# Optimization experiments

Measured on AMD Instinct MI355X. Metric: run time of the kernel, lower is better.

## Reference

```python
import math
import jax, jax.numpy as jnp
import numpy as np

B, N_COLS, CHANNELS, NUM_HEADS = 512, 128, 512, 8
D_HEAD = CHANNELS // NUM_HEADS


def setup_inputs() -> dict:
    key = jax.random.key(0)
    ks = jax.random.split(key, 9)
    s = 1.0 / math.sqrt(CHANNELS)
    x = jax.random.normal(ks[0], (B, N_COLS, CHANNELS), dtype=jnp.float32)
    Wq = jax.random.uniform(ks[1], (CHANNELS, CHANNELS), jnp.float32, -s, s)
    bq = jax.random.uniform(ks[2], (CHANNELS,), jnp.float32, -s, s)
    Wk = jax.random.uniform(ks[3], (CHANNELS, CHANNELS), jnp.float32, -s, s)
    bk = jax.random.uniform(ks[4], (CHANNELS,), jnp.float32, -s, s)
    Wv = jax.random.uniform(ks[5], (CHANNELS, CHANNELS), jnp.float32, -s, s)
    bv = jax.random.uniform(ks[6], (CHANNELS,), jnp.float32, -s, s)
    Wo = jax.random.uniform(ks[7], (CHANNELS, CHANNELS), jnp.float32, -s, s)
    bo = jax.random.uniform(ks[8], (CHANNELS,), jnp.float32, -s, s)
    return {"x": x, "Wq": Wq, "bq": bq, "Wk": Wk, "bk": bk,
            "Wv": Wv, "bv": bv, "Wo": Wo, "bo": bo}


def reference(x, Wq, bq, Wk, bk, Wv, bv, Wo, bo):
    b, n, c = x.shape
    h, d = NUM_HEADS, D_HEAD

    def split_heads(t):  # [b, n, c] -> [b, h, n, d]
        return t.reshape(b, n, h, d).transpose(0, 2, 1, 3)

    Q = split_heads(x @ Wq + bq)
    K = split_heads(x @ Wk + bk)
    V = split_heads(x @ Wv + bv)

    # raw scores [b, h, q, k]
    scores = jnp.einsum('bhqd,bhkd->bhqk', Q, K)
    # causal mask over columns; note: mask added BEFORE scaling by sqrt(d)
    causal = jnp.tril(jnp.ones((n, n), dtype=jnp.float32))
    mask = (1.0 - causal) * -100000.0
    attn = jax.nn.softmax((scores + mask) / math.sqrt(d), axis=-1)
    out = jnp.einsum('bhqk,bhkd->bhqd', attn, V)
    out = out.transpose(0, 2, 1, 3).reshape(b, n, c)
    return out @ Wo + bo
```

## Files before the change

### kernel.cpp

```cpp
#include <hip/hip_runtime.h>

typedef _Float16 f16;
typedef _Float16 half8 __attribute__((ext_vector_type(8)));
typedef _Float16 half4 __attribute__((ext_vector_type(4)));
typedef float f32x4 __attribute__((ext_vector_type(4)));

#define B_SZ 512
#define NQ   128
#define CH   512
#define NH   8
#define DH   64
#define MTOK (B_SZ*NQ)
#define KD   512

#define MFMA16(a,b,c) __builtin_amdgcn_mfma_f32_16x16x32_f16((a),(b),(c),0,0,0)

#define GLDS16(g,l) __builtin_amdgcn_global_load_lds( \
    (__attribute__((address_space(1))) void*)(g), \
    (__attribute__((address_space(3))) void*)(l), 16, 0, 0)

__global__ __launch_bounds__(256) void k_cvt(const float* __restrict__ x,
                                             f16* __restrict__ xb) {
  const int n8 = MTOK * KD / 8;
  int i = blockIdx.x * blockDim.x + threadIdx.x;
  const int stride = gridDim.x * blockDim.x;
  for (; i < n8; i += stride) {
    f32x4 a = ((const f32x4*)x)[2 * i];
    f32x4 b = ((const f32x4*)x)[2 * i + 1];
    half8 h;
    h[0] = (f16)a[0]; h[1] = (f16)a[1]; h[2] = (f16)a[2]; h[3] = (f16)a[3];
    h[4] = (f16)b[0]; h[5] = (f16)b[1]; h[6] = (f16)b[2]; h[7] = (f16)b[3];
    ((half8*)xb)[i] = h;
  }
}

__global__ __launch_bounds__(256) void k_wt(const float* __restrict__ Wq,
                                            const float* __restrict__ Wk,
                                            const float* __restrict__ Wv,
                                            const float* __restrict__ Wo,
                                            f16* __restrict__ wt) {
  const int n = blockIdx.x;
  const float* W = (n < 512) ? Wq : (n < 1024) ? Wk : (n < 1536) ? Wv : Wo;
  const int c = n & 511;
  for (int k = threadIdx.x; k < 512; k += blockDim.x)
    wt[n * 512 + k] = (f16)W[k * 512 + c];
}

__global__ __launch_bounds__(256, 4) void k_qkv(
    const f16* __restrict__ A, const f16* __restrict__ Bw,
    const float* __restrict__ bq, const float* __restrict__ bk,
    const float* __restrict__ bv,
    f16* __restrict__ qb, f16* __restrict__ kb, f16* __restrict__ vb) {
  __shared__ f16 la[128 * 32];
  __shared__ f16 lb[128 * 32];
  const int tid = threadIdx.x;
  const int w = tid >> 6, lane = tid & 63;
  const int ln = lane & 15, g = lane >> 4;
  const int wr = w >> 1, wc = w & 1;
  const int s = blockIdx.x >> 3;
  const int ml = s / 12;
  const int ntile = s - ml * 12;
  const int mtile = (blockIdx.x & 7) * 64 + ml;

  const int srow = w * 16 + (lane >> 2);
  const int scol = ((lane & 3) ^ ((lane >> 3) & 3)) * 8;
  const f16* gA = A + (mtile * 128 + srow) * KD + scol;
  const f16* gB = Bw + (ntile * 128 + srow) * KD + scol;
  f16* lA = la + w * 512;
  f16* lB = lb + w * 512;
  const int slotx = (g ^ ((ln >> 1) & 3)) * 8;

  f32x4 acc[4][4] = {};

  for (int kt = 0; kt < 16; ++kt) {
    const int k0 = kt * 32;
    GLDS16(gA + k0, lA);
    GLDS16(gA + 64 * KD + k0, lA + 2048);
    GLDS16(gB + k0, lB);
    GLDS16(gB + 64 * KD + k0, lB + 2048);
    __syncthreads();
    half8 af[4], bf[4];
#pragma unroll
    for (int m = 0; m < 4; ++m)
      af[m] = *(const half8*)(la + (wr * 64 + m * 16 + ln) * 32 + slotx);
#pragma unroll
    for (int n = 0; n < 4; ++n)
      bf[n] = *(const half8*)(lb + (wc * 64 + n * 16 + ln) * 32 + slotx);
#pragma unroll
    for (int m = 0; m < 4; ++m)
#pragma unroll
      for (int n = 0; n < 4; ++n)
        acc[m][n] = MFMA16(af[m], bf[n], acc[m][n]);
    __syncthreads();
  }

  const int b = mtile;
  const int colbase = ntile * 128 + wc * 64;
#pragma unroll
  for (int m = 0; m < 4; ++m) {
    const int nn0 = wr * 64 + m * 16 + g * 4;
#pragma unroll
    for (int n = 0; n < 4; ++n) {
      const int col = colbase + n * 16 + ln;
      const int which = col >> 9;
      const int c = col & 511;
      const int h = c >> 6, d = c & 63;
      const float bias = (which == 0) ? bq[c] : (which == 1) ? bk[c] : bv[c];
      if (which < 2) {
        f16* dst = ((which == 0) ? qb : kb) + ((b * NH + h) * NQ + nn0) * DH + d;
#pragma unroll
        for (int r = 0; r < 4; ++r)
          dst[r * DH] = (f16)(acc[m][n][r] + bias);
      } else {
        half4 v4;
#pragma unroll
        for (int r = 0; r < 4; ++r)
          v4[r] = (f16)(acc[m][n][r] + bias);
        *(half4*)(vb + ((b * NH + h) * DH + d) * NQ + nn0) = v4;
      }
    }
  }
}

__global__ __launch_bounds__(256, 2) void k_attn(
    const f16* __restrict__ qbuf, const f16* __restrict__ kbuf,
    const f16* __restrict__ vbuf, f16* __restrict__ ao) {
  __shared__ f16 kl[128 * 72];
  __shared__ f16 vl[64 * 136];
  __shared__ f16 pl[128 * 136];
  const int bh = blockIdx.x;
  const f16* Qp = qbuf + bh * (NQ * DH);
  const f16* Kp = kbuf + bh * (NQ * DH);
  const f16* Vp = vbuf + bh * (DH * NQ);
  const int tid = threadIdx.x;
  const int w = tid >> 6, lane = tid & 63;
  const int ln = lane & 15, g = lane >> 4;

#pragma unroll
  for (int i = 0; i < 4; ++i) {
    const int e = i * 2048 + tid * 8;
    *(half8*)(kl + (e >> 6) * 72 + (e & 63)) = *(const half8*)(Kp + e);
  }
#pragma unroll
  for (int i = 0; i < 4; ++i) {
    const int e = i * 2048 + tid * 8;
    *(half8*)(vl + (e >> 7) * 136 + (e & 127)) = *(const half8*)(Vp + e);
  }
  half8 qf[2][2];
#pragma unroll
  for (int m = 0; m < 2; ++m)
#pragma unroll
    for (int ks = 0; ks < 2; ++ks)
      qf[m][ks] = *(const half8*)(Qp + (w * 32 + m * 16 + ln) * DH + ks * 32 + g * 8);
  __syncthreads();

  f32x4 s[2][8] = {};
#pragma unroll
  for (int ks = 0; ks < 2; ++ks)
#pragma unroll
    for (int n = 0; n < 8; ++n) {
      half8 kf = *(const half8*)(kl + (n * 16 + ln) * 72 + ks * 32 + g * 8);
      s[0][n] = MFMA16(qf[0][ks], kf, s[0][n]);
      s[1][n] = MFMA16(qf[1][ks], kf, s[1][n]);
    }

  float inv[2][4];
#pragma unroll
  for (int m = 0; m < 2; ++m) {
#pragma unroll
    for (int r = 0; r < 4; ++r) {
      const int q = w * 32 + m * 16 + g * 4 + r;
      float z[8];
      float rm = -1e30f;
#pragma unroll
      for (int n = 0; n < 8; ++n) {
        const int col = n * 16 + ln;
        float zz = s[m][n][r] * 0.125f + ((col > q) ? -12500.0f : 0.0f);
        z[n] = zz;
        rm = fmaxf(rm, zz);
      }
      rm = fmaxf(rm, __shfl_xor(rm, 1));
      rm = fmaxf(rm, __shfl_xor(rm, 2));
      rm = fmaxf(rm, __shfl_xor(rm, 4));
      rm = fmaxf(rm, __shfl_xor(rm, 8));
      float rs = 0.f;
#pragma unroll
      for (int n = 0; n < 8; ++n) {
        const float p = __expf(z[n] - rm);
        rs += p;
        pl[q * 136 + n * 16 + ln] = (f16)p;
      }
      rs += __shfl_xor(rs, 1);
      rs += __shfl_xor(rs, 2);
      rs += __shfl_xor(rs, 4);
      rs += __shfl_xor(rs, 8);
      inv[m][r] = 1.0f / rs;
    }
  }

  f32x4 o[2][4] = {};
#pragma unroll
  for (int ks = 0; ks < 4; ++ks) {
    half8 pf0 = *(const half8*)(pl + (w * 32 + ln) * 136 + ks * 32 + g * 8);
    half8 pf1 = *(const half8*)(pl + (w * 32 + 16 + ln) * 136 + ks * 32 + g * 8);
#pragma unroll
    for (int n = 0; n < 4; ++n) {
      half8 vf = *(const half8*)(vl + (n * 16 + ln) * 136 + ks * 32 + g * 8);
      o[0][n] = MFMA16(pf0, vf, o[0][n]);
      o[1][n] = MFMA16(pf1, vf, o[1][n]);
    }
  }

  const int b = bh >> 3, h = bh & 7;
  f16* dst = ao + (b * NQ) * CH + h * DH;
#pragma unroll
  for (int m = 0; m < 2; ++m)
#pragma unroll
    for (int n = 0; n < 4; ++n)
#pragma unroll
      for (int r = 0; r < 4; ++r) {
        const int q = w * 32 + m * 16 + g * 4 + r;
        dst[q * CH + n * 16 + ln] = (f16)(o[m][n][r] * inv[m][r]);
      }
}

__global__ __launch_bounds__(256, 4) void k_out(
    const f16* __restrict__ A, const f16* __restrict__ Bw,
    const float* __restrict__ bo, float* __restrict__ out) {
  __shared__ f16 la[128 * 32];
  __shared__ f16 lb[128 * 32];
  const int tid = threadIdx.x;
  const int w = tid >> 6, lane = tid & 63;
  const int ln = lane & 15, g = lane >> 4;
  const int wr = w >> 1, wc = w & 1;
  const int s = blockIdx.x >> 3;
  const int ml = s >> 2;
  const int ntile = s & 3;
  const int mtile = (blockIdx.x & 7) * 64 + ml;

  const int srow = w * 16 + (lane >> 2);
  const int scol = ((lane & 3) ^ ((lane >> 3) & 3)) * 8;
  const f16* gA = A + (mtile * 128 + srow) * KD + scol;
  const f16* gB = Bw + (ntile * 128 + srow) * KD + scol;
  f16* lA = la + w * 512;
  f16* lB = lb + w * 512;
  const int slotx = (g ^ ((ln >> 1) & 3)) * 8;

  f32x4 acc[4][4] = {};

  for (int kt = 0; kt < 16; ++kt) {
    const int k0 = kt * 32;
    GLDS16(gA + k0, lA);
    GLDS16(gA + 64 * KD + k0, lA + 2048);
    GLDS16(gB + k0, lB);
    GLDS16(gB + 64 * KD + k0, lB + 2048);
    __syncthreads();
    half8 af[4], bf[4];
#pragma unroll
    for (int m = 0; m < 4; ++m)
      af[m] = *(const half8*)(la + (wr * 64 + m * 16 + ln) * 32 + slotx);
#pragma unroll
    for (int n = 0; n < 4; ++n)
      bf[n] = *(const half8*)(lb + (wc * 64 + n * 16 + ln) * 32 + slotx);
#pragma unroll
    for (int m = 0; m < 4; ++m)
#pragma unroll
      for (int n = 0; n < 4; ++n)
        acc[m][n] = MFMA16(af[m], bf[n], acc[m][n]);
    __syncthreads();
  }

  const int colbase = ntile * 128 + wc * 64;
#pragma unroll
  for (int m = 0; m < 4; ++m) {
    const int tok0 = mtile * 128 + wr * 64 + m * 16 + g * 4;
#pragma unroll
    for (int n = 0; n < 4; ++n) {
      const int col = colbase + n * 16 + ln;
      const float bias = bo[col];
      float* dst = out + tok0 * CH + col;
#pragma unroll
      for (int r = 0; r < 4; ++r)
        dst[r * CH] = acc[m][n][r] + bias;
    }
  }
}

extern "C" void kernel_launch(void* const* d_in, const int* in_sizes, int n_in,
                              void* d_out, int out_size, void* d_ws, size_t ws_size,
                              hipStream_t stream) {
  (void)in_sizes; (void)n_in; (void)out_size; (void)ws_size;
  const float* x  = (const float*)d_in[0];
  const float* Wq = (const float*)d_in[1];
  const float* bq = (const float*)d_in[2];
  const float* Wk = (const float*)d_in[3];
  const float* bk = (const float*)d_in[4];
  const float* Wv = (const float*)d_in[5];
  const float* bv = (const float*)d_in[6];
  const float* Wo = (const float*)d_in[7];
  const float* bo = (const float*)d_in[8];
  float* out = (float*)d_out;

  char* ws = (char*)d_ws;
  const size_t SZ = (size_t)MTOK * KD * sizeof(f16);
  f16* xb = (f16*)(ws);
  f16* qb = (f16*)(ws + SZ);
  f16* kb = (f16*)(ws + 2 * SZ);
  f16* vb = (f16*)(ws + 3 * SZ);
  f16* wt = (f16*)(ws + 4 * SZ);
  f16* ao = xb;

  k_cvt<<<2048, 256, 0, stream>>>(x, xb);
  k_wt<<<2048, 256, 0, stream>>>(Wq, Wk, Wv, Wo, wt);
  k_qkv<<<6144, 256, 0, stream>>>(xb, wt, bq, bk, bv, qb, kb, vb);
  k_attn<<<4096, 256, 0, stream>>>(qb, kb, vb, ao);
  k_out<<<2048, 256, 0, stream>>>(ao, wt + 1536 * KD, bo, out);
}
```

Before: 309.5 us.

## Triple-buffer GEMM LDS loads and merge conversion kernels into one launch

Replaces the single-buffered GEMM main loop in the QKV and output projections with a three-stage LDS ring. Global-to-LDS loads run two k-steps ahead, each step waits on a vmcnt and a single barrier instead of two syncthreads, and MFMA sections are raised with s_setprio. It also fuses the x conversion and weight transpose kernels into one launch. The cost is three times the LDS per block (48KB), which may reduce occupancy under launch_bounds(256,4).

```diff
diff --git a/kernel.cpp b/kernel.cpp
--- a/kernel.cpp
+++ b/kernel.cpp
@@ -19,31 +19,92 @@
     (__attribute__((address_space(1))) void*)(g), \
     (__attribute__((address_space(3))) void*)(l), 16, 0, 0)
 
-__global__ __launch_bounds__(256) void k_cvt(const float* __restrict__ x,
-                                             f16* __restrict__ xb) {
-  const int n8 = MTOK * KD / 8;
-  int i = blockIdx.x * blockDim.x + threadIdx.x;
-  const int stride = gridDim.x * blockDim.x;
-  for (; i < n8; i += stride) {
-    f32x4 a = ((const f32x4*)x)[2 * i];
-    f32x4 b = ((const f32x4*)x)[2 * i + 1];
-    half8 h;
-    h[0] = (f16)a[0]; h[1] = (f16)a[1]; h[2] = (f16)a[2]; h[3] = (f16)a[3];
-    h[4] = (f16)b[0]; h[5] = (f16)b[1]; h[6] = (f16)b[2]; h[7] = (f16)b[3];
-    ((half8*)xb)[i] = h;
-  }
-}
-
-__global__ __launch_bounds__(256) void k_wt(const float* __restrict__ Wq,
-                                            const float* __restrict__ Wk,
-                                            const float* __restrict__ Wv,
-                                            const float* __restrict__ Wo,
-                                            f16* __restrict__ wt) {
-  const int n = blockIdx.x;
-  const float* W = (n < 512) ? Wq : (n < 1024) ? Wk : (n < 1536) ? Wv : Wo;
-  const int c = n & 511;
-  for (int k = threadIdx.x; k < 512; k += blockDim.x)
-    wt[n * 512 + k] = (f16)W[k * 512 + c];
+__global__ __launch_bounds__(256) void k_prep(
+    const float* __restrict__ x,
+    const float* __restrict__ Wq, const float* __restrict__ Wk,
+    const float* __restrict__ Wv, const float* __restrict__ Wo,
+    f16* __restrict__ xb, f16* __restrict__ wt) {
+  const int bid = blockIdx.x;
+  if (bid < 512) {
+    for (int e = threadIdx.x; e < 2048; e += 256) {
+      const int n = bid * 4 + (e >> 9);
+      const int k = e & 511;
+      const float* W = (n < 512) ? Wq : (n < 1024) ? Wk : (n < 1536) ? Wv : Wo;
+      wt[n * 512 + k] = (f16)W[k * 512 + (n & 511)];
+    }
+  } else {
+    const int n8 = MTOK * KD / 8;
+    int i = (bid - 512) * 256 + threadIdx.x;
+    const int stride = 2048 * 256;
+    for (; i < n8; i += stride) {
+      f32x4 a = ((const f32x4*)x)[2 * i];
+      f32x4 b = ((const f32x4*)x)[2 * i + 1];
+      half8 h;
+      h[0] = (f16)a[0]; h[1] = (f16)a[1]; h[2] = (f16)a[2]; h[3] = (f16)a[3];
+      h[4] = (f16)b[0]; h[5] = (f16)b[1]; h[6] = (f16)b[2]; h[7] = (f16)b[3];
+      ((half8*)xb)[i] = h;
+    }
+  }
+}
+
+__device__ __forceinline__ void step128(const f16* pa, const f16* pb,
+                                        int roA, int roB, f32x4 (&acc)[4][4]) {
+  half8 af[4], bf[4];
+#pragma unroll
+  for (int m = 0; m < 4; ++m) af[m] = *(const half8*)(pa + roA + m * 512);
+#pragma unroll
+  for (int n = 0; n < 4; ++n) bf[n] = *(const half8*)(pb + roB + n * 512);
+  __builtin_amdgcn_s_setprio(1);
+#pragma unroll
+  for (int m = 0; m < 4; ++m)
+#pragma unroll
+    for (int n = 0; n < 4; ++n)
+      acc[m][n] = MFMA16(af[m], bf[n], acc[m][n]);
+  __builtin_amdgcn_s_setprio(0);
+}
+
+__device__ __forceinline__ void gemm128_pf(
+    const f16* __restrict__ Ag, const f16* __restrict__ Bg,
+    f16* la, f16* lb, f32x4 (&acc)[4][4]) {
+  const int tid = threadIdx.x;
+  const int w = tid >> 6, lane = tid & 63;
+  const int ln = lane & 15, g = lane >> 4;
+  const int wr = w >> 1, wc = w & 1;
+  const int srow = w * 16 + (lane >> 2);
+  const int scol = ((lane & 3) ^ ((lane >> 3) & 3)) * 8;
+  const f16* gA = Ag + srow * KD + scol;
+  const f16* gB = Bg + srow * KD + scol;
+  const int w512 = w * 512;
+  f16 *pa0 = la, *pa1 = la + 4096, *pa2 = la + 8192;
+  f16 *pb0 = lb, *pb1 = lb + 4096, *pb2 = lb + 8192;
+  const int slotx = (g ^ ((ln >> 1) & 3)) * 8;
+  const int roA = (wr * 64 + ln) * 32 + slotx;
+  const int roB = (wc * 64 + ln) * 32 + slotx;
+
+  GLDS16(gA,           pa0 + w512); GLDS16(gA + 64*KD,      pa0 + w512 + 2048);
+  GLDS16(gB,           pb0 + w512); GLDS16(gB + 64*KD,      pb0 + w512 + 2048);
+  GLDS16(gA + 32,      pa1 + w512); GLDS16(gA + 64*KD + 32, pa1 + w512 + 2048);
+  GLDS16(gB + 32,      pb1 + w512); GLDS16(gB + 64*KD + 32, pb1 + w512 + 2048);
+  asm volatile("s_waitcnt vmcnt(4)" ::: "memory");
+  __builtin_amdgcn_s_barrier();
+
+  const f16* gAs = gA + 64;
+  const f16* gBs = gB + 64;
+#pragma unroll 1
+  for (int t = 0; t < 14; ++t) {
+    GLDS16(gAs, pa2 + w512); GLDS16(gAs + 64*KD, pa2 + w512 + 2048);
+    GLDS16(gBs, pb2 + w512); GLDS16(gBs + 64*KD, pb2 + w512 + 2048);
+    gAs += 32; gBs += 32;
+    step128(pa0, pb0, roA, roB, acc);
+    asm volatile("s_waitcnt vmcnt(4)" ::: "memory");
+    __builtin_amdgcn_s_barrier();
+    f16* t1 = pa0; pa0 = pa1; pa1 = pa2; pa2 = t1;
+    f16* t2 = pb0; pb0 = pb1; pb1 = pb2; pb2 = t2;
+  }
+  step128(pa0, pb0, roA, roB, acc);
+  asm volatile("s_waitcnt vmcnt(0)" ::: "memory");
+  __builtin_amdgcn_s_barrier();
+  step128(pa1, pb1, roA, roB, acc);
 }
 
 __global__ __launch_bounds__(256, 4) void k_qkv(
@@ -51,8 +112,8 @@
     const float* __restrict__ bq, const float* __restrict__ bk,
     const float* __restrict__ bv,
     f16* __restrict__ qb, f16* __restrict__ kb, f16* __restrict__ vb) {
-  __shared__ f16 la[128 * 32];
-  __shared__ f16 lb[128 * 32];
+  __shared__ f16 la[3 * 4096];
+  __shared__ f16 lb[3 * 4096];
   const int tid = threadIdx.x;
   const int w = tid >> 6, lane = tid & 63;
   const int ln = lane & 15, g = lane >> 4;
@@ -62,37 +123,8 @@
   const int ntile = s - ml * 12;
   const int mtile = (blockIdx.x & 7) * 64 + ml;
 
-  const int srow = w * 16 + (lane >> 2);
-  const int scol = ((lane & 3) ^ ((lane >> 3) & 3)) * 8;
-  const f16* gA = A + (mtile * 128 + srow) * KD + scol;
-  const f16* gB = Bw + (ntile * 128 + srow) * KD + scol;
-  f16* lA = la + w * 512;
-  f16* lB = lb + w * 512;
-  const int slotx = (g ^ ((ln >> 1) & 3)) * 8;
-
   f32x4 acc[4][4] = {};
-
-  for (int kt = 0; kt < 16; ++kt) {
-    const int k0 = kt * 32;
-    GLDS16(gA + k0, lA);
-    GLDS16(gA + 64 * KD + k0, lA + 2048);
-    GLDS16(gB + k0, lB);
-    GLDS16(gB + 64 * KD + k0, lB + 2048);
-    __syncthreads();
-    half8 af[4], bf[4];
-#pragma unroll
-    for (int m = 0; m < 4; ++m)
-      af[m] = *(const half8*)(la + (wr * 64 + m * 16 + ln) * 32 + slotx);
-#pragma unroll
-    for (int n = 0; n < 4; ++n)
-      bf[n] = *(const half8*)(lb + (wc * 64 + n * 16 + ln) * 32 + slotx);
-#pragma unroll
-    for (int m = 0; m < 4; ++m)
-#pragma unroll
-      for (int n = 0; n < 4; ++n)
-        acc[m][n] = MFMA16(af[m], bf[n], acc[m][n]);
-    __syncthreads();
-  }
+  gemm128_pf(A + mtile * 128 * KD, Bw + ntile * 128 * KD, la, lb, acc);
 
   const int b = mtile;
   const int colbase = ntile * 128 + wc * 64;
@@ -227,8 +259,8 @@
 __global__ __launch_bounds__(256, 4) void k_out(
     const f16* __restrict__ A, const f16* __restrict__ Bw,
     const float* __restrict__ bo, float* __restrict__ out) {
-  __shared__ f16 la[128 * 32];
-  __shared__ f16 lb[128 * 32];
+  __shared__ f16 la[3 * 4096];
+  __shared__ f16 lb[3 * 4096];
   const int tid = threadIdx.x;
   const int w = tid >> 6, lane = tid & 63;
   const int ln = lane & 15, g = lane >> 4;
@@ -238,37 +270,8 @@
   const int ntile = s & 3;
   const int mtile = (blockIdx.x & 7) * 64 + ml;
 
-  const int srow = w * 16 + (lane >> 2);
-  const int scol = ((lane & 3) ^ ((lane >> 3) & 3)) * 8;
-  const f16* gA = A + (mtile * 128 + srow) * KD + scol;
-  const f16* gB = Bw + (ntile * 128 + srow) * KD + scol;
-  f16* lA = la + w * 512;
-  f16* lB = lb + w * 512;
-  const int slotx = (g ^ ((ln >> 1) & 3)) * 8;
-
   f32x4 acc[4][4] = {};
-
-  for (int kt = 0; kt < 16; ++kt) {
-    const int k0 = kt * 32;
-    GLDS16(gA + k0, lA);
-    GLDS16(gA + 64 * KD + k0, lA + 2048);
-    GLDS16(gB + k0, lB);
-    GLDS16(gB + 64 * KD + k0, lB + 2048);
-    __syncthreads();
-    half8 af[4], bf[4];
-#pragma unroll
-    for (int m = 0; m < 4; ++m)
-      af[m] = *(const half8*)(la + (wr * 64 + m * 16 + ln) * 32 + slotx);
-#pragma unroll
-    for (int n = 0; n < 4; ++n)
-      bf[n] = *(const half8*)(lb + (wc * 64 + n * 16 + ln) * 32 + slotx);
-#pragma unroll
-    for (int m = 0; m < 4; ++m)
-#pragma unroll
-      for (int n = 0; n < 4; ++n)
-        acc[m][n] = MFMA16(af[m], bf[n], acc[m][n]);
-    __syncthreads();
-  }
+  gemm128_pf(A + mtile * 128 * KD, Bw + ntile * 128 * KD, la, lb, acc);
 
   const int colbase = ntile * 128 + wc * 64;
 #pragma unroll
@@ -310,8 +313,7 @@
   f16* wt = (f16*)(ws + 4 * SZ);
   f16* ao = xb;
 
-  k_cvt<<<2048, 256, 0, stream>>>(x, xb);
-  k_wt<<<2048, 256, 0, stream>>>(Wq, Wk, Wv, Wo, wt);
+  k_prep<<<2560, 256, 0, stream>>>(x, Wq, Wk, Wv, Wo, xb, wt);
   k_qkv<<<6144, 256, 0, stream>>>(xb, wt, bq, bk, bv, qb, kb, vb);
   k_attn<<<4096, 256, 0, stream>>>(qb, kb, vb, ao);
   k_out<<<2048, 256, 0, stream>>>(ao, wt + 1536 * KD, bo, out);
```

After: 333.7 us. +7.8%, slower.
